# Optimization experiments

Measured on AMD Instinct MI355X. Metric: run time of the kernel, lower is better.

Reference implementation:

```python
import jax, jax.numpy as jnp
import numpy as np

RX, RY = 10, 10  # box filter half-widths (Angle == 0 path)


def setup_inputs() -> dict:
    key = jax.random.key(0)
    x = jax.random.normal(key, (8, 1, 2048, 2048), dtype=jnp.float32)
    # Angle == 0: constant all-ones box kernel (1,1,2rx+1,2ry+1), a fixed buffer
    kernelx = jnp.ones((1, 1, 2 * RX + 1, 2 * RY + 1), dtype=jnp.float32)
    return {"x": x, "kernelx": kernelx}


def reference(x, kernelx):
    # circular pad: H by rx (top/bottom), W by ry (left/right), matching
    # F.pad(input, (ry, ry, rx, rx), mode='circular')
    xp = jnp.pad(x, ((0, 0), (0, 0), (RX, RX), (RY, RY)), mode="wrap")
    # valid conv with the box kernel -> output has the original HxW
    out = jax.lax.conv_general_dilated(
        xp, kernelx,
        window_strides=(1, 1),
        padding="VALID",
        dimension_numbers=("NCHW", "OIHW", "NCHW"),
    )
    return out
```

## Files before the change

### kernel.cpp

```cpp
#include <hip/hip_runtime.h>


#define HH 2048
#define WW 2048
#define RAD 10
#define DIAM 21
#define TH 32
#define TW 128
#define NC4 38
#define SSTR 156

typedef float nfloat4 __attribute__((ext_vector_type(4)));

__global__ __launch_bounds__(256) void box_filter_v4(
    const float* __restrict__ x, float* __restrict__ out) {
  __shared__ float sCS[TH * SSTR];

  const int n = blockIdx.z;
  const int h0 = blockIdx.y * TH;
  const int w0 = blockIdx.x * TW;
  const float* __restrict__ xp = x + (size_t)n * (HH * WW);
  float* __restrict__ op = out + (size_t)n * (HH * WW);
  const int tid = threadIdx.x;

  if (tid < NC4 * 2) {
    const int c4 = tid % NC4;
    const int g = tid / NC4;
    const int gc = (w0 - 12 + 4 * c4) & (WW - 1);
    const int rbase = h0 + 16 * g - RAD;
    nfloat4 v[36];
#pragma unroll
    for (int k = 0; k < 36; ++k)
      v[k] = *(const nfloat4*)(xp + (size_t)((rbase + k) & (HH - 1)) * WW + gc);
    nfloat4 s = v[0];
#pragma unroll
    for (int k = 1; k < DIAM; ++k) s += v[k];
    *(nfloat4*)&sCS[(16 * g) * SSTR + 4 * c4] = s;
#pragma unroll
    for (int i = 1; i < 16; ++i) {
      s += v[i + 20] - v[i - 1];
      *(nfloat4*)&sCS[(16 * g + i) * SSTR + 4 * c4] = s;
    }
  }
  __syncthreads();

  {
    const int r = tid >> 3;
    const int cg = tid & 7;
    const float* row = &sCS[r * SSTR + 16 * cg];
    float* orow = &op[(size_t)(h0 + r) * WW + w0 + 16 * cg];
    __align__(16) float w[40];
#pragma unroll
    for (int k = 0; k < 10; ++k)
      *(nfloat4*)&w[4 * k] = *(const nfloat4*)&row[4 * k];
    float s = w[2];
#pragma unroll
    for (int k = 3; k <= 22; ++k) s += w[k];
    float o[16];
    o[0] = s;
#pragma unroll
    for (int j = 1; j < 16; ++j) {
      s += w[j + 22] - w[j + 1];
      o[j] = s;
    }
#pragma unroll
    for (int q = 0; q < 4; ++q) {
      nfloat4 ov = {o[4 * q], o[4 * q + 1], o[4 * q + 2], o[4 * q + 3]};
      __builtin_nontemporal_store(ov, (nfloat4*)&orow[4 * q]);
    }
  }
}

extern "C" void kernel_launch(void* const* d_in, const int* in_sizes, int n_in,
                              void* d_out, int out_size, void* d_ws, size_t ws_size,
                              hipStream_t stream) {
  const float* x = (const float*)d_in[0];
  float* out = (float*)d_out;
  dim3 grid(WW / TW, HH / TH, 8);
  dim3 block(256);
  hipLaunchKernelGGL(box_filter_v4, grid, block, 0, stream, x, out);
}
```

Measured before the change: 285.5 us.

## Stream rows with running vertical column sums and double-buffered LDS row

Replaces the per-tile two-pass approach (load a 36-row halo, build vertical sums in LDS, then do horizontal sums) with a streaming kernel. Each block walks 128 rows of a 512-wide strip and keeps a running vertical column sum in registers, using prefetch rings to add the entering row and subtract the leaving one. Each row's column sums go through a double-buffered LDS row, and the horizontal window is computed per row with a barrier per row. This cuts vertical halo over-read, but it adds 128 barriers per block, shrinks the grid, uses plain rather than nontemporal stores, and may not hide latency as well.

```diff
diff --git a/kernel.cpp b/kernel.cpp
--- a/kernel.cpp
+++ b/kernel.cpp
@@ -5,68 +5,80 @@
 #define WW 2048
 #define RAD 10
 #define DIAM 21
-#define TH 32
-#define TW 128
-#define NC4 38
-#define SSTR 156
+#define TW 512
+#define CH 128
+#define NQ 134
+#define SW (NQ * 4)
+#define VT 134
+#define HT 128
 
 typedef float nfloat4 __attribute__((ext_vector_type(4)));
 
-__global__ __launch_bounds__(256) void box_filter_v4(
+__global__ __launch_bounds__(192) void box_filter_v6(
     const float* __restrict__ x, float* __restrict__ out) {
-  __shared__ float sCS[TH * SSTR];
+  __shared__ float sbuf[2][SW];
 
   const int n = blockIdx.z;
-  const int h0 = blockIdx.y * TH;
+  const int r0 = blockIdx.y * CH;
   const int w0 = blockIdx.x * TW;
   const float* __restrict__ xp = x + (size_t)n * (HH * WW);
   float* __restrict__ op = out + (size_t)n * (HH * WW);
-  const int tid = threadIdx.x;
+  const int t = threadIdx.x;
 
-  if (tid < NC4 * 2) {
-    const int c4 = tid % NC4;
-    const int g = tid / NC4;
-    const int gc = (w0 - 12 + 4 * c4) & (WW - 1);
-    const int rbase = h0 + 16 * g - RAD;
-    nfloat4 v[36];
+  const int gc = (w0 - 12 + 4 * t) & (WW - 1);
+  const float* __restrict__ colp = xp + gc;
+
+#define LOADQ(r) \
+  (*(const nfloat4*)(colp + (size_t)(((r) + 2 * HH) & (HH - 1)) * WW))
+
+  nfloat4 colsum = {0.f, 0.f, 0.f, 0.f};
+  nfloat4 ldn[7];
+  nfloat4 ldo[3];
+
+  if (t < VT) {
 #pragma unroll
-    for (int k = 0; k < 36; ++k)
-      v[k] = *(const nfloat4*)(xp + (size_t)((rbase + k) & (HH - 1)) * WW + gc);
-    nfloat4 s = v[0];
+    for (int i = 0; i < 7; ++i) ldn[i] = LOADQ(r0 + 10 + i);
 #pragma unroll
-    for (int k = 1; k < DIAM; ++k) s += v[k];
-    *(nfloat4*)&sCS[(16 * g) * SSTR + 4 * c4] = s;
+    for (int i = 0; i < 3; ++i) ldo[i] = LOADQ(r0 + i - 11);
 #pragma unroll
-    for (int i = 1; i < 16; ++i) {
-      s += v[i + 20] - v[i - 1];
-      *(nfloat4*)&sCS[(16 * g + i) * SSTR + 4 * c4] = s;
-    }
+    for (int j = 0; j < DIAM; ++j) colsum += LOADQ(r0 + j - 11);
   }
-  __syncthreads();
 
-  {
-    const int r = tid >> 3;
-    const int cg = tid & 7;
-    const float* row = &sCS[r * SSTR + 16 * cg];
-    float* orow = &op[(size_t)(h0 + r) * WW + w0 + 16 * cg];
-    __align__(16) float w[40];
+  bool done = false;
+  for (int g = 0; g < 7 && !done; ++g) {
 #pragma unroll
-    for (int k = 0; k < 10; ++k)
-      *(nfloat4*)&w[4 * k] = *(const nfloat4*)&row[4 * k];
-    float s = w[2];
+    for (int j = 0; j < DIAM; ++j) {
+      const int rof = DIAM * g + j;
+      if (rof >= CH) { done = true; break; }
+      const int rr = r0 + rof;
+
+      if (t < VT) {
+        nfloat4 nv = ldn[j % 7];
+        ldn[j % 7] = LOADQ(rr + 17);
+        nfloat4 ov = ldo[j % 3];
+        ldo[j % 3] = LOADQ(rr - 8);
+        colsum += nv - ov;
+        *(nfloat4*)&sbuf[rr & 1][4 * t] = colsum;
+      }
+      asm volatile("s_waitcnt lgkmcnt(0)" ::: "memory");
+      __builtin_amdgcn_s_barrier();
+
+      if (t < HT) {
+        const float* b = &sbuf[rr & 1][4 * t];
+        float w[28];
 #pragma unroll
-    for (int k = 3; k <= 22; ++k) s += w[k];
-    float o[16];
-    o[0] = s;
+        for (int k = 0; k < 7; ++k)
+          *(nfloat4*)&w[4 * k] = *(const nfloat4*)&b[4 * k];
+        float s = w[2];
 #pragma unroll
-    for (int j = 1; j < 16; ++j) {
-      s += w[j + 22] - w[j + 1];
-      o[j] = s;
-    }
-#pragma unroll
-    for (int q = 0; q < 4; ++q) {
-      nfloat4 ov = {o[4 * q], o[4 * q + 1], o[4 * q + 2], o[4 * q + 3]};
-      __builtin_nontemporal_store(ov, (nfloat4*)&orow[4 * q]);
+        for (int k = 3; k <= 22; ++k) s += w[k];
+        nfloat4 o;
+        o.x = s;
+        s += w[23] - w[2]; o.y = s;
+        s += w[24] - w[3]; o.z = s;
+        s += w[25] - w[4]; o.w = s;
+        *(nfloat4*)&op[(size_t)rr * WW + w0 + 4 * t] = o;
+      }
     }
   }
 }
@@ -76,7 +88,7 @@
                               hipStream_t stream) {
   const float* x = (const float*)d_in[0];
   float* out = (float*)d_out;
-  dim3 grid(WW / TW, HH / TH, 8);
-  dim3 block(256);
-  hipLaunchKernelGGL(box_filter_v4, grid, block, 0, stream, x, out);
+  dim3 grid(WW / TW, HH / CH, 8);
+  dim3 block(192);
+  hipLaunchKernelGGL(box_filter_v6, grid, block, 0, stream, x, out);
 }
```

Measured after the change: 369.7 us. 29.5% more time.

## Stage input tile into LDS via global_load_lds using all threads

Applied to the files above, without the earlier changes.

Before, 76 threads each loaded 36 float4 rows into registers. Now all 256 threads cooperatively copy the padded 52x38-float4 input tile straight into LDS with global_load_lds, which bypasses VGPRs. The vertical sliding sum then reads from LDS. This spreads the load work across the whole block and frees registers, at the cost of about 31.6KB of extra shared memory, which may lower occupancy. The output stores also switch from nontemporal to regular stores.

```diff
diff --git a/kernel.cpp b/kernel.cpp
--- a/kernel.cpp
+++ b/kernel.cpp
@@ -7,13 +7,18 @@
 #define DIAM 21
 #define TH 32
 #define TW 128
-#define NC4 38
+#define NQ 38
+#define RROWS (TH + 20)
+#define RQ (RROWS * NQ)
 #define SSTR 156
 
 typedef float nfloat4 __attribute__((ext_vector_type(4)));
+typedef const __attribute__((address_space(1))) void* gp_t;
+typedef __attribute__((address_space(3))) void* lp_t;
 
-__global__ __launch_bounds__(256) void box_filter_v4(
+__global__ __launch_bounds__(256) void box_filter_v7(
     const float* __restrict__ x, float* __restrict__ out) {
+  __shared__ float sRAW[RQ * 4];
   __shared__ float sCS[TH * SSTR];
 
   const int n = blockIdx.z;
@@ -23,22 +28,38 @@
   float* __restrict__ op = out + (size_t)n * (HH * WW);
   const int tid = threadIdx.x;
 
-  if (tid < NC4 * 2) {
-    const int c4 = tid % NC4;
-    const int g = tid / NC4;
-    const int gc = (w0 - 12 + 4 * c4) & (WW - 1);
-    const int rbase = h0 + 16 * g - RAD;
-    nfloat4 v[36];
+  {
+    const int wbase = tid & ~63;
 #pragma unroll
-    for (int k = 0; k < 36; ++k)
-      v[k] = *(const nfloat4*)(xp + (size_t)((rbase + k) & (HH - 1)) * WW + gc);
-    nfloat4 s = v[0];
+    for (int it = 0; it < 8; ++it) {
+      const int idx = it * 256 + tid;
+      if (idx < RQ) {
+        const int r = idx / NQ;
+        const int c = idx - r * NQ;
+        const int grow = (h0 - RAD + r) & (HH - 1);
+        const int gcol = (w0 - 12 + 4 * c) & (WW - 1);
+        const float* src = xp + (size_t)grow * WW + gcol;
+        float* dst = &sRAW[(size_t)(it * 256 + wbase) * 4];
+        __builtin_amdgcn_global_load_lds((gp_t)(uintptr_t)src,
+                                         (lp_t)(uintptr_t)dst, 16, 0, 0);
+      }
+    }
+  }
+  __syncthreads();
+
+  if (tid < NQ * 2) {
+    const int c4 = tid % NQ;
+    const int g = tid / NQ;
+    const float* base = &sRAW[((16 * g) * NQ + c4) * 4];
+    nfloat4 s = *(const nfloat4*)base;
 #pragma unroll
-    for (int k = 1; k < DIAM; ++k) s += v[k];
+    for (int k = 1; k < DIAM; ++k)
+      s += *(const nfloat4*)(base + k * (NQ * 4));
     *(nfloat4*)&sCS[(16 * g) * SSTR + 4 * c4] = s;
 #pragma unroll
     for (int i = 1; i < 16; ++i) {
-      s += v[i + 20] - v[i - 1];
+      s += *(const nfloat4*)(base + (i + 20) * (NQ * 4)) -
+           *(const nfloat4*)(base + (i - 1) * (NQ * 4));
       *(nfloat4*)&sCS[(16 * g + i) * SSTR + 4 * c4] = s;
     }
   }
@@ -66,7 +87,7 @@
 #pragma unroll
     for (int q = 0; q < 4; ++q) {
       nfloat4 ov = {o[4 * q], o[4 * q + 1], o[4 * q + 2], o[4 * q + 3]};
-      __builtin_nontemporal_store(ov, (nfloat4*)&orow[4 * q]);
+      *(nfloat4*)&orow[4 * q] = ov;
     }
   }
 }
@@ -78,5 +99,5 @@
   float* out = (float*)d_out;
   dim3 grid(WW / TW, HH / TH, 8);
   dim3 block(256);
-  hipLaunchKernelGGL(box_filter_v4, grid, block, 0, stream, x, out);
+  hipLaunchKernelGGL(box_filter_v7, grid, block, 0, stream, x, out);
 }
```

Result: faster. 239.5 us (-16.1%).
